# Optimization experiments

Hardware: AMD Instinct MI355X
Metric: run time of the kernel (lower is better)

The kernel has to match this reference:

```python
import jax, jax.numpy as jnp
import numpy as np

# Deterministic, fully-vectorized JAX version of the augmentation pipeline
# (labels=None branch). Randomness comes from a fixed PRNG key so the
# reference is reproducible. All per-sample PIL/CPU loops in the original
# are replaced by batched on-device ops: affine warp + hflip (geometric),
# brightness/contrast/saturation jitter (color), 3x3 gaussian blur,
# random erasing, GridMask, final clamp to [0,1].


def _affine_warp(x, key):
    """Batched inverse-mapped bilinear affine warp. x: [B,C,H,W]."""
    B, C, H, W = x.shape
    k1, k2, k3, k4 = jax.random.split(key, 4)
    deg = jnp.pi / 180.0
    ang = jax.random.uniform(k1, (B,), minval=-25.0, maxval=25.0) * deg
    shr = jax.random.uniform(k2, (B,), minval=-15.0, maxval=15.0) * deg
    scl = jax.random.uniform(k3, (B,), minval=0.85, maxval=1.15)
    trn = jax.random.uniform(k4, (B, 2), minval=-0.15, maxval=0.15)
    tx = trn[:, 0] * W
    ty = trn[:, 1] * H
    c, s = jnp.cos(ang), jnp.sin(ang)
    t = jnp.tan(shr)
    # inverse map (output pixel -> input pixel): shear^-1 @ rot^-1 / scale
    m00 = (c - t * (-s)) / scl
    m01 = (s - t * c) / scl
    m10 = (-s) / scl
    m11 = c / scl
    M = jnp.stack([jnp.stack([m00, m01], -1), jnp.stack([m10, m11], -1)], -2)  # [B,2,2]
    # centered pixel coordinate grid [2,H,W] (x, y)
    ys = jnp.arange(H, dtype=x.dtype) - (H - 1) / 2.0
    xs = jnp.arange(W, dtype=x.dtype) - (W - 1) / 2.0
    gy, gx = jnp.meshgrid(ys, xs, indexing='ij')
    grid = jnp.stack([gx, gy], 0)  # [2,H,W]
    src = jnp.einsum('bij,jhw->bihw', M, grid)  # [B,2,H,W]
    sx = src[:, 0] - tx[:, None, None] + (W - 1) / 2.0
    sy = src[:, 1] - ty[:, None, None] + (H - 1) / 2.0

    def sample_one(img, sx1, sy1):  # img [C,H,W]; sx1,sy1 [H,W]
        x0 = jnp.floor(sx1)
        y0 = jnp.floor(sy1)
        wx = sx1 - x0
        wy = sy1 - y0
        x0i = x0.astype(jnp.int32)
        y0i = y0.astype(jnp.int32)

        def g(yi, xi):
            valid = ((xi >= 0) & (xi < W) & (yi >= 0) & (yi < H)).astype(img.dtype)
            return img[:, jnp.clip(yi, 0, H - 1), jnp.clip(xi, 0, W - 1)] * valid

        return (g(y0i, x0i) * (1 - wx) * (1 - wy)
                + g(y0i, x0i + 1) * wx * (1 - wy)
                + g(y0i + 1, x0i) * (1 - wx) * wy
                + g(y0i + 1, x0i + 1) * wx * wy)

    return jax.vmap(sample_one)(x, sx, sy)


def _color_jitter(x, key):
    B = x.shape[0]
    kb, kc, ks = jax.random.split(key, 3)
    b = jax.random.uniform(kb, (B, 1, 1, 1), minval=0.7, maxval=1.3)
    c = jax.random.uniform(kc, (B, 1, 1, 1), minval=0.7, maxval=1.3)
    s = jax.random.uniform(ks, (B, 1, 1, 1), minval=0.8, maxval=1.2)
    x = x * b  # brightness
    mean = jnp.mean(x, axis=(1, 2, 3), keepdims=True)
    x = (x - mean) * c + mean  # contrast
    luma = jnp.array([0.299, 0.587, 0.114], x.dtype)
    gray = jnp.einsum('bchw,c->bhw', x, luma)[:, None]  # [B,1,H,W]
    x = gray + (x - gray) * s  # saturation
    return x


def _gaussian_blur3(x):
    C = x.shape[1]
    k1 = jnp.array([0.25, 0.5, 0.25], x.dtype)
    kern = jnp.outer(k1, k1)  # 3x3
    kern = jnp.tile(kern[None, None], (C, 1, 1, 1))  # [C,1,3,3] depthwise
    return jax.lax.conv_general_dilated(x, kern, (1, 1), 'SAME',
                                        feature_group_count=C,
                                        dimension_numbers=('NCHW', 'OIHW', 'NCHW'))


def _random_erasing(x, key):
    B, C, H, W = x.shape
    ka, kr, kt, kl, kv, kp = jax.random.split(key, 6)
    area = jax.random.uniform(ka, (B,), minval=0.02, maxval=0.1) * H * W
    ratio = jax.random.uniform(kr, (B,), minval=0.3, maxval=3.0)
    eh = jnp.clip(jnp.sqrt(area * ratio), 1, H)
    ew = jnp.clip(jnp.sqrt(area / ratio), 1, W)
    top = jax.random.uniform(kt, (B,)) * (H - eh)
    left = jax.random.uniform(kl, (B,)) * (W - ew)
    rows = jnp.arange(H, dtype=x.dtype)[None, :]
    cols = jnp.arange(W, dtype=x.dtype)[None, :]
    rmask = (rows >= top[:, None]) & (rows < (top + eh)[:, None])  # [B,H]
    cmask = (cols >= left[:, None]) & (cols < (left + ew)[:, None])  # [B,W]
    box = (rmask[:, None, :, None] & cmask[:, None, None, :])  # [B,1,H,W]
    fill = jax.random.uniform(kv, x.shape, dtype=x.dtype)  # value='random'
    apply = jax.random.bernoulli(kp, 0.3, (B, 1, 1, 1))
    return jnp.where(box & apply, fill, x)


def _grid_mask(x, key):
    B, C, H, W = x.shape
    kd, kp = jax.random.split(key)
    d = jnp.floor(jax.random.uniform(kd, (B,), minval=8.0, maxval=32.0))
    l = jnp.floor(d * 0.6)
    rows = jnp.arange(H, dtype=x.dtype)[None, :]
    cols = jnp.arange(W, dtype=x.dtype)[None, :]
    rh = jnp.mod(rows, d[:, None]) < l[:, None]  # [B,H]
    rw = jnp.mod(cols, d[:, None]) < l[:, None]  # [B,W]
    hole = rh[:, None, :, None] & rw[:, None, None, :]  # [B,1,H,W]
    apply = jax.random.bernoulli(kp, 0.3, (B, 1, 1, 1))
    return jnp.where(hole & apply, jnp.zeros_like(x), x)


def setup_inputs() -> dict:
    key = jax.random.key(0)
    x = jax.random.uniform(key, (2048, 3, 64, 64), dtype=jnp.float32)
    return {"x": x}


def reference(x) -> jnp.ndarray:
    B = x.shape[0]
    key = jax.random.key(42)
    kg, kf, kc, kb, ke, km = jax.random.split(key, 6)
    # geometric: affine warp + random horizontal flip (p=0.6)
    x = _affine_warp(x, kg)
    flip = jax.random.bernoulli(kf, 0.6, (B, 1, 1, 1))
    x = jnp.where(flip, x[..., ::-1], x)
    # color jitter
    x = _color_jitter(x, kc)
    # gaussian blur, applied per-sample with p=0.3
    blur = jax.random.bernoulli(kb, 0.3, (B, 1, 1, 1))
    x = jnp.where(blur, _gaussian_blur3(x), x)
    # random erasing
    x = _random_erasing(x, ke)
    # grid mask
    x = _grid_mask(x, km)
    return jnp.clip(x, 0.0, 1.0)
```

## Files before the change

### kernel.cpp

```cpp
#include <hip/hip_runtime.h>
#include <stdint.h>
#include <math.h>

#pragma clang fp contract(off)

struct KeyPair { uint32_t hi, lo; };
struct KTab { KeyPair k[17]; };

__host__ __device__ __forceinline__ uint32_t rotl32(uint32_t x, int r) {
  return (x << r) | (x >> (32 - r));
}

__host__ __device__ __forceinline__ void threefry2x32(uint32_t k0, uint32_t k1,
                                                      uint32_t x0, uint32_t x1,
                                                      uint32_t& o0, uint32_t& o1) {
  const uint32_t ks0 = k0, ks1 = k1, ks2 = k0 ^ k1 ^ 0x1BD11BDAu;
  x0 += ks0; x1 += ks1;
#define TF_R(r) { x0 += x1; x1 = rotl32(x1, (r)); x1 ^= x0; }
  TF_R(13) TF_R(15) TF_R(26) TF_R(6)
  x0 += ks1; x1 += ks2 + 1u;
  TF_R(17) TF_R(29) TF_R(16) TF_R(24)
  x0 += ks2; x1 += ks0 + 2u;
  TF_R(13) TF_R(15) TF_R(26) TF_R(6)
  x0 += ks0; x1 += ks1 + 3u;
  TF_R(17) TF_R(29) TF_R(16) TF_R(24)
  x0 += ks1; x1 += ks2 + 4u;
  TF_R(13) TF_R(15) TF_R(26) TF_R(6)
  x0 += ks2; x1 += ks0 + 5u;
#undef TF_R
  o0 = x0; o1 = x1;
}

__host__ __device__ __forceinline__ uint32_t jax_rbits32(KeyPair k, uint32_t i) {
  uint32_t a, b; threefry2x32(k.hi, k.lo, 0u, i, a, b);
  return a ^ b;
}

__host__ __device__ __forceinline__ KeyPair jax_split_child(KeyPair k, uint32_t j) {
  uint32_t a, b; threefry2x32(k.hi, k.lo, 0u, j, a, b);
  KeyPair r; r.hi = a; r.lo = b; return r;
}

__host__ __device__ __forceinline__ float bits_to_unit(uint32_t bits) {
  uint32_t fb = (bits >> 9) | 0x3F800000u;
  return __builtin_bit_cast(float, fb) - 1.0f;
}

__device__ __forceinline__ float map_u(float u, float mn, float mx) {
  return fmaxf(mn, u * (mx - mn) + mn);
}

__device__ __forceinline__ void gload_lds16(const float* gsrc, float* ldst) {
  __builtin_amdgcn_global_load_lds(
      (const __attribute__((address_space(1))) unsigned int*)gsrc,
      (__attribute__((address_space(3))) unsigned int*)ldst,
      16, 0, 0);
}

struct SP {
  float m00, m01, m10, m11, txp, typ;
  float bb, cc, ssat;
  float topv, t2, leftv, l2;
  float dG, lG;
  int flip, doblur, apply_e, apply_g;
};

__global__ __launch_bounds__(512, 4) void aug_kernel(const float* __restrict__ in,
                                                     float* __restrict__ out,
                                                     KTab KT, KeyPair kv, int B) {
  const int b = blockIdx.x;
  const int tid = threadIdx.x;
  __shared__ float simg[3 * 64 * 64];
  __shared__ float uarr[17];
  __shared__ SP sp;
  __shared__ unsigned long long mgrid, merow, mecol;
  __shared__ float red[8];

  const float* __restrict__ inb = in + (size_t)b * 12288;

  {
    const int wv = tid >> 6;
    const int lane = tid & 63;
#pragma unroll
    for (int it = 0; it < 6; ++it) {
      const int base = it * 2048 + wv * 256;
      gload_lds16(inb + base + 4 * lane, &simg[base]);
    }
  }

  if (tid < 17) {
    KeyPair k = KT.k[tid];
    uint32_t i = (tid == 3) ? 2u * (uint32_t)b
               : (tid == 4) ? 2u * (uint32_t)b + 1u
               : (uint32_t)b;
    uarr[tid] = bits_to_unit(jax_rbits32(k, i));
  }
  __syncthreads();

  if (tid == 0) {
    const float DEG = 0.017453292519943295f;
    float ang = map_u(uarr[0], -25.f, 25.f) * DEG;
    float shr = map_u(uarr[1], -15.f, 15.f) * DEG;
    float scl = map_u(uarr[2], 0.85f, 1.15f);
    sp.txp = map_u(uarr[3], -0.15f, 0.15f) * 64.f;
    sp.typ = map_u(uarr[4], -0.15f, 0.15f) * 64.f;
    float cA = cosf(ang), sA = sinf(ang), tS = tanf(shr);
    sp.m00 = (cA - tS * (-sA)) / scl;
    sp.m01 = (sA - tS * cA) / scl;
    sp.m10 = (-sA) / scl;
    sp.m11 = cA / scl;
    sp.flip = uarr[5] < 0.6f;
    sp.bb = map_u(uarr[6], 0.7f, 1.3f);
    sp.cc = map_u(uarr[7], 0.7f, 1.3f);
    sp.ssat = map_u(uarr[8], 0.8f, 1.2f);
    sp.doblur = uarr[9] < 0.3f;
    float area = map_u(uarr[10], 0.02f, 0.1f);
    area = area * 64.f;
    area = area * 64.f;
    float ratio = map_u(uarr[11], 0.3f, 3.0f);
    float eh = fminf(fmaxf(sqrtf(area * ratio), 1.f), 64.f);
    float ew = fminf(fmaxf(sqrtf(area / ratio), 1.f), 64.f);
    float topv = uarr[12] * (64.f - eh);
    float leftv = uarr[13] * (64.f - ew);
    sp.topv = topv; sp.t2 = topv + eh;
    sp.leftv = leftv; sp.l2 = leftv + ew;
    sp.apply_e = uarr[14] < 0.3f;
    float dG = floorf(map_u(uarr[15], 8.f, 32.f));
    sp.dG = dG;
    sp.lG = floorf(dG * 0.6f);
    sp.apply_g = uarr[16] < 0.3f;
  }
  __syncthreads();

  if (tid < 64) {
    float rf = (float)tid;
    unsigned long long g = __ballot(fmodf(rf, sp.dG) < sp.lG);
    unsigned long long er = __ballot((rf >= sp.topv) & (rf < sp.t2));
    unsigned long long ec = __ballot((rf >= sp.leftv) & (rf < sp.l2));
    if (tid == 0) { mgrid = g; merow = er; mecol = ec; }
  }
  __syncthreads();

  const float m00 = sp.m00, m01 = sp.m01, m10 = sp.m10, m11 = sp.m11;
  const float txp = sp.txp, typ = sp.typ;
  const float bb = sp.bb, cc = sp.cc, ssat = sp.ssat;
  const int flip = sp.flip, doblur = sp.doblur;
  const int apply_e = sp.apply_e, apply_g = sp.apply_g;
  const unsigned long long mg = mgrid, mer = merow, mec = mecol;

  float lsum = 0.f;
  for (int c = 0; c < 3; ++c) {
    float* plane = &simg[c * 4096];
    float vv[8];
#pragma unroll
    for (int it = 0; it < 8; ++it) {
      const int p = tid + it * 512;
      const int h = p >> 6;
      const int w = p & 63;
      const int wsrc = flip ? (63 - w) : w;
      const float gx = (float)wsrc - 31.5f;
      const float gy = (float)h - 31.5f;
      const float sx = (m00 * gx + m01 * gy) - txp + 31.5f;
      const float sy = (m10 * gx + m11 * gy) - typ + 31.5f;
      const float fx0 = floorf(sx), fy0 = floorf(sy);
      const float wx = sx - fx0, wy = sy - fy0;
      const int x0 = (int)fx0, y0 = (int)fy0;
      auto tap = [&](int yy, int xx) -> float {
        const bool v = (xx >= 0) & (xx < 64) & (yy >= 0) & (yy < 64);
        const int yc = yy < 0 ? 0 : (yy > 63 ? 63 : yy);
        const int xc = xx < 0 ? 0 : (xx > 63 ? 63 : xx);
        return v ? plane[yc * 64 + xc] : 0.f;
      };
      float v = tap(y0, x0)         * (1.f - wx) * (1.f - wy)
              + tap(y0, x0 + 1)     * wx         * (1.f - wy)
              + tap(y0 + 1, x0)     * (1.f - wx) * wy
              + tap(y0 + 1, x0 + 1) * wx         * wy;
      vv[it] = v;
      lsum += v;
    }
    if (c == 2) {
      float wsum = lsum;
      for (int off = 32; off > 0; off >>= 1) wsum += __shfl_down(wsum, off);
      if ((tid & 63) == 0) red[tid >> 6] = wsum;
    }
    __syncthreads();
#pragma unroll
    for (int it = 0; it < 8; ++it) plane[tid + it * 512] = vv[it];
  }
  __syncthreads();

  const float mean = (bb * (red[0] + red[1] + red[2] + red[3] +
                            red[4] + red[5] + red[6] + red[7])) / 12288.f;
  const float Ac = ssat * cc * bb;
  const float Gc = (1.f - ssat) * cc * bb;
  const float mprime = mean * (1.f - cc);

#pragma unroll 1
  for (int it = 0; it < 2; ++it) {
    const int qq = tid + it * 512;
    const int h = qq >> 4;
    const int w0 = (qq & 15) * 4;
    float px[3][4];
    if (doblur) {
#pragma unroll
      for (int c = 0; c < 3; ++c) {
        float win[3][6];
#pragma unroll
        for (int r = 0; r < 3; ++r) {
          const int hh = h - 1 + r;
          if (hh >= 0 && hh <= 63) {
            const float* row = &simg[c * 4096 + hh * 64];
            const float4 c4 = *(const float4*)&row[w0];
            win[r][1] = c4.x; win[r][2] = c4.y; win[r][3] = c4.z; win[r][4] = c4.w;
            win[r][0] = (w0 > 0)  ? row[w0 - 1] : 0.f;
            win[r][5] = (w0 < 60) ? row[w0 + 4] : 0.f;
          } else {
            win[r][0] = win[r][1] = win[r][2] = win[r][3] = win[r][4] = win[r][5] = 0.f;
          }
        }
#pragma unroll
        for (int j = 0; j < 4; ++j) {
          const float h0 = 0.25f * win[0][j] + 0.5f * win[0][j + 1] + 0.25f * win[0][j + 2];
          const float h1 = 0.25f * win[1][j] + 0.5f * win[1][j + 1] + 0.25f * win[1][j + 2];
          const float h2 = 0.25f * win[2][j] + 0.5f * win[2][j + 1] + 0.25f * win[2][j + 2];
          px[c][j] = 0.25f * h0 + 0.5f * h1 + 0.25f * h2;
        }
      }
    } else {
#pragma unroll
      for (int c = 0; c < 3; ++c) {
        const float4 c4 = *(const float4*)&simg[c * 4096 + h * 64 + w0];
        px[c][0] = c4.x; px[c][1] = c4.y; px[c][2] = c4.z; px[c][3] = c4.w;
      }
    }
    const float rowe = (h == 0 || h == 63) ? 0.75f : 1.f;
    const bool erow_b = apply_e && ((mer >> h) & 1ull);
    const bool grow_b = apply_g && ((mg >> h) & 1ull);
    float o[3][4];
#pragma unroll
    for (int j = 0; j < 4; ++j) {
      const int w = w0 + j;
      const float gray = 0.299f * px[0][j] + 0.587f * px[1][j] + 0.114f * px[2][j];
      float moff = mprime;
      if (doblur) {
        const float cole = (w == 0 || w == 63) ? 0.75f : 1.f;
        moff = mprime * (rowe * cole);
      }
      const bool do_er = erow_b && ((mec >> w) & 1ull);
      const bool do_gr = grow_b && ((mg >> w) & 1ull);
#pragma unroll
      for (int c = 0; c < 3; ++c) {
        float v = Ac * px[c][j] + Gc * gray + moff;
        if (do_er) {
          const uint32_t idx = ((uint32_t)(b * 3 + c) << 12) | (uint32_t)(h << 6) | (uint32_t)w;
          v = bits_to_unit(jax_rbits32(kv, idx));
        }
        if (do_gr) v = 0.f;
        o[c][j] = fminf(fmaxf(v, 0.f), 1.f);
      }
    }
#pragma unroll
    for (int c = 0; c < 3; ++c) {
      float4 st; st.x = o[c][0]; st.y = o[c][1]; st.z = o[c][2]; st.w = o[c][3];
      *(float4*)&out[(size_t)b * 12288 + c * 4096 + h * 64 + w0] = st;
    }
  }
}

extern "C" void kernel_launch(void* const* d_in, const int* in_sizes, int n_in,
                              void* d_out, int out_size, void* d_ws, size_t ws_size,
                              hipStream_t stream) {
  (void)n_in; (void)out_size; (void)d_ws; (void)ws_size;
  const float* x = (const float*)d_in[0];
  float* out = (float*)d_out;
  const int B = in_sizes[0] / (3 * 64 * 64);
  if (B <= 0) return;

  KeyPair root; root.hi = 0u; root.lo = 42u;
  KeyPair kg = jax_split_child(root, 0);
  KeyPair kf = jax_split_child(root, 1);
  KeyPair kc = jax_split_child(root, 2);
  KeyPair kb = jax_split_child(root, 3);
  KeyPair ke = jax_split_child(root, 4);
  KeyPair km = jax_split_child(root, 5);

  KTab KT;
  KT.k[0]  = jax_split_child(kg, 0);
  KT.k[1]  = jax_split_child(kg, 1);
  KT.k[2]  = jax_split_child(kg, 2);
  KT.k[3]  = jax_split_child(kg, 3);
  KT.k[4]  = KT.k[3];
  KT.k[5]  = kf;
  KT.k[6]  = jax_split_child(kc, 0);
  KT.k[7]  = jax_split_child(kc, 1);
  KT.k[8]  = jax_split_child(kc, 2);
  KT.k[9]  = kb;
  KT.k[10] = jax_split_child(ke, 0);
  KT.k[11] = jax_split_child(ke, 1);
  KT.k[12] = jax_split_child(ke, 2);
  KT.k[13] = jax_split_child(ke, 3);
  KT.k[14] = jax_split_child(ke, 5);
  KT.k[15] = jax_split_child(km, 0);
  KT.k[16] = jax_split_child(km, 1);
  KeyPair kv = jax_split_child(ke, 4);

  aug_kernel<<<dim3(B), dim3(512), 0, stream>>>(x, out, KT, kv, B);
}
```

Measured before the change: 185.3 us.

## Use zero-padded LDS image layout and fuse per-channel warp into single pass

Stores each channel in LDS with a one-pixel zero border and an odd row stride, so bilinear taps and blur windows need no bounds checks and see fewer bank conflicts. The warp now computes the coordinates once and samples all three channels, keeping results in registers and dropping the per-channel barriers. When no blur is applied, output is written straight from registers without going back through LDS. Random-parameter setup moves to one wavefront using shuffles, and global loads go through registers instead of the direct global-to-LDS path. The cost is higher register pressure (24 live warp values per thread) despite the raised occupancy hint, plus padding-based clamp logic that must exactly match the original out-of-range behaviour.

New measurement: 258.0 us. 39.2% more time.

```diff
diff --git a/kernel.cpp b/kernel.cpp
--- a/kernel.cpp
+++ b/kernel.cpp
@@ -50,94 +50,99 @@
   return fmaxf(mn, u * (mx - mn) + mn);
 }
 
-__device__ __forceinline__ void gload_lds16(const float* gsrc, float* ldst) {
-  __builtin_amdgcn_global_load_lds(
-      (const __attribute__((address_space(1))) unsigned int*)gsrc,
-      (__attribute__((address_space(3))) unsigned int*)ldst,
-      16, 0, 0);
-}
-
 struct SP {
   float m00, m01, m10, m11, txp, typ;
   float bb, cc, ssat;
-  float topv, t2, leftv, l2;
-  float dG, lG;
   int flip, doblur, apply_e, apply_g;
 };
 
-__global__ __launch_bounds__(512, 4) void aug_kernel(const float* __restrict__ in,
+#define RS  65
+#define PLS 4360
+
+__global__ __launch_bounds__(512, 6) void aug_kernel(const float* __restrict__ in,
                                                      float* __restrict__ out,
                                                      KTab KT, KeyPair kv, int B) {
   const int b = blockIdx.x;
   const int tid = threadIdx.x;
-  __shared__ float simg[3 * 64 * 64];
-  __shared__ float uarr[17];
+  __shared__ float simg[3 * PLS];
   __shared__ SP sp;
   __shared__ unsigned long long mgrid, merow, mecol;
   __shared__ float red[8];
 
   const float* __restrict__ inb = in + (size_t)b * 12288;
 
-  {
-    const int wv = tid >> 6;
-    const int lane = tid & 63;
-#pragma unroll
-    for (int it = 0; it < 6; ++it) {
-      const int base = it * 2048 + wv * 256;
-      gload_lds16(inb + base + 4 * lane, &simg[base]);
-    }
-  }
-
-  if (tid < 17) {
-    KeyPair k = KT.k[tid];
-    uint32_t i = (tid == 3) ? 2u * (uint32_t)b
-               : (tid == 4) ? 2u * (uint32_t)b + 1u
-               : (uint32_t)b;
-    uarr[tid] = bits_to_unit(jax_rbits32(k, i));
-  }
-  __syncthreads();
-
-  if (tid == 0) {
+  float4 st[6];
+#pragma unroll
+  for (int it = 0; it < 6; ++it) st[it] = ((const float4*)inb)[tid + it * 512];
+
+  if (tid < 64) {
+    float myu = 0.f;
+    if (tid < 17) {
+      KeyPair k = KT.k[tid];
+      uint32_t i = (tid == 3) ? 2u * (uint32_t)b
+                 : (tid == 4) ? 2u * (uint32_t)b + 1u
+                 : (uint32_t)b;
+      myu = bits_to_unit(jax_rbits32(k, i));
+    }
+    float u[17];
+#pragma unroll
+    for (int j = 0; j < 17; ++j) u[j] = __shfl(myu, j);
+
     const float DEG = 0.017453292519943295f;
-    float ang = map_u(uarr[0], -25.f, 25.f) * DEG;
-    float shr = map_u(uarr[1], -15.f, 15.f) * DEG;
-    float scl = map_u(uarr[2], 0.85f, 1.15f);
-    sp.txp = map_u(uarr[3], -0.15f, 0.15f) * 64.f;
-    sp.typ = map_u(uarr[4], -0.15f, 0.15f) * 64.f;
-    float cA = cosf(ang), sA = sinf(ang), tS = tanf(shr);
-    sp.m00 = (cA - tS * (-sA)) / scl;
-    sp.m01 = (sA - tS * cA) / scl;
-    sp.m10 = (-sA) / scl;
-    sp.m11 = cA / scl;
-    sp.flip = uarr[5] < 0.6f;
-    sp.bb = map_u(uarr[6], 0.7f, 1.3f);
-    sp.cc = map_u(uarr[7], 0.7f, 1.3f);
-    sp.ssat = map_u(uarr[8], 0.8f, 1.2f);
-    sp.doblur = uarr[9] < 0.3f;
-    float area = map_u(uarr[10], 0.02f, 0.1f);
+    const float ang = map_u(u[0], -25.f, 25.f) * DEG;
+    const float shr = map_u(u[1], -15.f, 15.f) * DEG;
+    const float scl = map_u(u[2], 0.85f, 1.15f);
+    const float t_x = map_u(u[3], -0.15f, 0.15f) * 64.f;
+    const float t_y = map_u(u[4], -0.15f, 0.15f) * 64.f;
+    const float cA = cosf(ang), sA = sinf(ang), tS = tanf(shr);
+    float area = map_u(u[10], 0.02f, 0.1f);
     area = area * 64.f;
     area = area * 64.f;
-    float ratio = map_u(uarr[11], 0.3f, 3.0f);
-    float eh = fminf(fmaxf(sqrtf(area * ratio), 1.f), 64.f);
-    float ew = fminf(fmaxf(sqrtf(area / ratio), 1.f), 64.f);
-    float topv = uarr[12] * (64.f - eh);
-    float leftv = uarr[13] * (64.f - ew);
-    sp.topv = topv; sp.t2 = topv + eh;
-    sp.leftv = leftv; sp.l2 = leftv + ew;
-    sp.apply_e = uarr[14] < 0.3f;
-    float dG = floorf(map_u(uarr[15], 8.f, 32.f));
-    sp.dG = dG;
-    sp.lG = floorf(dG * 0.6f);
-    sp.apply_g = uarr[16] < 0.3f;
-  }
-  __syncthreads();
-
-  if (tid < 64) {
-    float rf = (float)tid;
-    unsigned long long g = __ballot(fmodf(rf, sp.dG) < sp.lG);
-    unsigned long long er = __ballot((rf >= sp.topv) & (rf < sp.t2));
-    unsigned long long ec = __ballot((rf >= sp.leftv) & (rf < sp.l2));
-    if (tid == 0) { mgrid = g; merow = er; mecol = ec; }
+    const float ratio = map_u(u[11], 0.3f, 3.0f);
+    const float eh = fminf(fmaxf(sqrtf(area * ratio), 1.f), 64.f);
+    const float ew = fminf(fmaxf(sqrtf(area / ratio), 1.f), 64.f);
+    const float topv = u[12] * (64.f - eh);
+    const float leftv = u[13] * (64.f - ew);
+    const float dG = floorf(map_u(u[15], 8.f, 32.f));
+    const float lG = floorf(dG * 0.6f);
+
+    const float rf = (float)tid;
+    const unsigned long long g  = __ballot(fmodf(rf, dG) < lG);
+    const unsigned long long er = __ballot((rf >= topv) & (rf < (topv + eh)));
+    const unsigned long long ec = __ballot((rf >= leftv) & (rf < (leftv + ew)));
+    if (tid == 0) {
+      sp.m00 = (cA - tS * (-sA)) / scl;
+      sp.m01 = (sA - tS * cA) / scl;
+      sp.m10 = (-sA) / scl;
+      sp.m11 = cA / scl;
+      sp.txp = t_x; sp.typ = t_y;
+      sp.flip = u[5] < 0.6f;
+      sp.bb = map_u(u[6], 0.7f, 1.3f);
+      sp.cc = map_u(u[7], 0.7f, 1.3f);
+      sp.ssat = map_u(u[8], 0.8f, 1.2f);
+      sp.doblur = u[9] < 0.3f;
+      sp.apply_e = u[14] < 0.3f;
+      sp.apply_g = u[16] < 0.3f;
+      mgrid = g; merow = er; mecol = ec;
+    }
+  } else if (tid < 328) {
+    const int z = tid - 64;
+    int a;
+    if (z < 65)       a = z;
+    else if (z < 200) a = 4160 + z;
+    else              a = (z - 199) * RS;
+#pragma unroll
+    for (int c = 0; c < 3; ++c) simg[c * PLS + a] = 0.f;
+  }
+
+#pragma unroll
+  for (int it = 0; it < 6; ++it) {
+    const int f = it * 2048 + tid * 4;
+    const int c = f >> 12;
+    const int r = (f >> 6) & 63;
+    const int cc = f & 63;
+    float* d = &simg[c * PLS + (r + 1) * RS + cc + 1];
+    d[0] = st[it].x; d[1] = st[it].y; d[2] = st[it].z; d[3] = st[it].w;
   }
   __syncthreads();
 
@@ -148,44 +153,37 @@
   const int apply_e = sp.apply_e, apply_g = sp.apply_g;
   const unsigned long long mg = mgrid, mer = merow, mec = mecol;
 
+  float vv[3][8];
   float lsum = 0.f;
-  for (int c = 0; c < 3; ++c) {
-    float* plane = &simg[c * 4096];
-    float vv[8];
-#pragma unroll
-    for (int it = 0; it < 8; ++it) {
-      const int p = tid + it * 512;
-      const int h = p >> 6;
-      const int w = p & 63;
-      const int wsrc = flip ? (63 - w) : w;
-      const float gx = (float)wsrc - 31.5f;
-      const float gy = (float)h - 31.5f;
-      const float sx = (m00 * gx + m01 * gy) - txp + 31.5f;
-      const float sy = (m10 * gx + m11 * gy) - typ + 31.5f;
-      const float fx0 = floorf(sx), fy0 = floorf(sy);
-      const float wx = sx - fx0, wy = sy - fy0;
-      const int x0 = (int)fx0, y0 = (int)fy0;
-      auto tap = [&](int yy, int xx) -> float {
-        const bool v = (xx >= 0) & (xx < 64) & (yy >= 0) & (yy < 64);
-        const int yc = yy < 0 ? 0 : (yy > 63 ? 63 : yy);
-        const int xc = xx < 0 ? 0 : (xx > 63 ? 63 : xx);
-        return v ? plane[yc * 64 + xc] : 0.f;
-      };
-      float v = tap(y0, x0)         * (1.f - wx) * (1.f - wy)
-              + tap(y0, x0 + 1)     * wx         * (1.f - wy)
-              + tap(y0 + 1, x0)     * (1.f - wx) * wy
-              + tap(y0 + 1, x0 + 1) * wx         * wy;
-      vv[it] = v;
+#pragma unroll
+  for (int it = 0; it < 8; ++it) {
+    const int p = tid + it * 512;
+    const int h = p >> 6;
+    const int w = p & 63;
+    const int wsrc = flip ? (63 - w) : w;
+    const float gx = (float)wsrc - 31.5f;
+    const float gy = (float)h - 31.5f;
+    float sx = (m00 * gx + m01 * gy) - txp + 31.5f;
+    float sy = (m10 * gx + m11 * gy) - typ + 31.5f;
+    sx = fminf(fmaxf(sx, -1.f), 64.f);
+    sy = fminf(fmaxf(sy, -1.f), 64.f);
+    const float fx0 = floorf(sx), fy0 = floorf(sy);
+    const float wx = sx - fx0, wy = sy - fy0;
+    const float omx = 1.f - wx, omy = 1.f - wy;
+    const float w00 = omx * omy, w01 = wx * omy, w10 = omx * wy, w11 = wx * wy;
+    const int a = ((int)fy0 + 1) * RS + (int)fx0 + 1;
+#pragma unroll
+    for (int c = 0; c < 3; ++c) {
+      const float* t = &simg[c * PLS + a];
+      const float v = t[0] * w00 + t[1] * w01 + t[RS] * w10 + t[RS + 1] * w11;
+      vv[c][it] = v;
       lsum += v;
     }
-    if (c == 2) {
-      float wsum = lsum;
-      for (int off = 32; off > 0; off >>= 1) wsum += __shfl_down(wsum, off);
-      if ((tid & 63) == 0) red[tid >> 6] = wsum;
-    }
-    __syncthreads();
-#pragma unroll
-    for (int it = 0; it < 8; ++it) plane[tid + it * 512] = vv[it];
+  }
+  {
+    float wsum = lsum;
+    for (int off = 32; off > 0; off >>= 1) wsum += __shfl_down(wsum, off);
+    if ((tid & 63) == 0) red[tid >> 6] = wsum;
   }
   __syncthreads();
 
@@ -194,29 +192,50 @@
   const float Ac = ssat * cc * bb;
   const float Gc = (1.f - ssat) * cc * bb;
   const float mprime = mean * (1.f - cc);
-
+  float* __restrict__ ob = out + (size_t)b * 12288;
+
+  if (!doblur) {
+#pragma unroll
+    for (int it = 0; it < 8; ++it) {
+      const int p = tid + it * 512;
+      const int h = p >> 6, w = p & 63;
+      const bool do_er = apply_e && ((mer >> h) & 1ull) && ((mec >> w) & 1ull);
+      const bool do_gr = apply_g && ((mg >> h) & 1ull) && ((mg >> w) & 1ull);
+      const float gray = 0.299f * vv[0][it] + 0.587f * vv[1][it] + 0.114f * vv[2][it];
+#pragma unroll
+      for (int c = 0; c < 3; ++c) {
+        float v = Ac * vv[c][it] + Gc * gray + mprime;
+        if (do_er) {
+          const uint32_t idx = ((uint32_t)(b * 3 + c) << 12) | (uint32_t)p;
+          v = bits_to_unit(jax_rbits32(kv, idx));
+        }
+        if (do_gr) v = 0.f;
+        ob[c * 4096 + p] = fminf(fmaxf(v, 0.f), 1.f);
+      }
+    }
+  } else {
+#pragma unroll
+    for (int it = 0; it < 8; ++it) {
+      const int p = tid + it * 512;
+      const int a = ((p >> 6) + 1) * RS + (p & 63) + 1;
+#pragma unroll
+      for (int c = 0; c < 3; ++c) simg[c * PLS + a] = vv[c][it];
+    }
+    __syncthreads();
 #pragma unroll 1
-  for (int it = 0; it < 2; ++it) {
-    const int qq = tid + it * 512;
-    const int h = qq >> 4;
-    const int w0 = (qq & 15) * 4;
-    float px[3][4];
-    if (doblur) {
+    for (int it = 0; it < 2; ++it) {
+      const int qq = tid + it * 512;
+      const int h = qq >> 4;
+      const int w0 = (qq & 15) * 4;
+      float px[3][4];
 #pragma unroll
       for (int c = 0; c < 3; ++c) {
         float win[3][6];
 #pragma unroll
         for (int r = 0; r < 3; ++r) {
-          const int hh = h - 1 + r;
-          if (hh >= 0 && hh <= 63) {
-            const float* row = &simg[c * 4096 + hh * 64];
-            const float4 c4 = *(const float4*)&row[w0];
-            win[r][1] = c4.x; win[r][2] = c4.y; win[r][3] = c4.z; win[r][4] = c4.w;
-            win[r][0] = (w0 > 0)  ? row[w0 - 1] : 0.f;
-            win[r][5] = (w0 < 60) ? row[w0 + 4] : 0.f;
-          } else {
-            win[r][0] = win[r][1] = win[r][2] = win[r][3] = win[r][4] = win[r][5] = 0.f;
-          }
+          const float* row = &simg[c * PLS + (h + r) * RS + w0];
+#pragma unroll
+          for (int k = 0; k < 6; ++k) win[r][k] = row[k];
         }
 #pragma unroll
         for (int j = 0; j < 4; ++j) {
@@ -226,43 +245,34 @@
           px[c][j] = 0.25f * h0 + 0.5f * h1 + 0.25f * h2;
         }
       }
-    } else {
+      const float rowe = (h == 0 || h == 63) ? 0.75f : 1.f;
+      const bool erow_b = apply_e && ((mer >> h) & 1ull);
+      const bool grow_b = apply_g && ((mg >> h) & 1ull);
+      float o[3][4];
+#pragma unroll
+      for (int j = 0; j < 4; ++j) {
+        const int w = w0 + j;
+        const float gray = 0.299f * px[0][j] + 0.587f * px[1][j] + 0.114f * px[2][j];
+        const float cole = (w == 0 || w == 63) ? 0.75f : 1.f;
+        const float moff = mprime * (rowe * cole);
+        const bool do_er = erow_b && ((mec >> w) & 1ull);
+        const bool do_gr = grow_b && ((mg >> w) & 1ull);
+#pragma unroll
+        for (int c = 0; c < 3; ++c) {
+          float v = Ac * px[c][j] + Gc * gray + moff;
+          if (do_er) {
+            const uint32_t idx = ((uint32_t)(b * 3 + c) << 12) | (uint32_t)(h << 6) | (uint32_t)w;
+            v = bits_to_unit(jax_rbits32(kv, idx));
+          }
+          if (do_gr) v = 0.f;
+          o[c][j] = fminf(fmaxf(v, 0.f), 1.f);
+        }
+      }
 #pragma unroll
       for (int c = 0; c < 3; ++c) {
-        const float4 c4 = *(const float4*)&simg[c * 4096 + h * 64 + w0];
-        px[c][0] = c4.x; px[c][1] = c4.y; px[c][2] = c4.z; px[c][3] = c4.w;
+        float4 stv; stv.x = o[c][0]; stv.y = o[c][1]; stv.z = o[c][2]; stv.w = o[c][3];
+        *(float4*)&ob[c * 4096 + h * 64 + w0] = stv;
       }
-    }
-    const float rowe = (h == 0 || h == 63) ? 0.75f : 1.f;
-    const bool erow_b = apply_e && ((mer >> h) & 1ull);
-    const bool grow_b = apply_g && ((mg >> h) & 1ull);
-    float o[3][4];
-#pragma unroll
-    for (int j = 0; j < 4; ++j) {
-      const int w = w0 + j;
-      const float gray = 0.299f * px[0][j] + 0.587f * px[1][j] + 0.114f * px[2][j];
-      float moff = mprime;
-      if (doblur) {
-        const float cole = (w == 0 || w == 63) ? 0.75f : 1.f;
-        moff = mprime * (rowe * cole);
-      }
-      const bool do_er = erow_b && ((mec >> w) & 1ull);
-      const bool do_gr = grow_b && ((mg >> w) & 1ull);
-#pragma unroll
-      for (int c = 0; c < 3; ++c) {
-        float v = Ac * px[c][j] + Gc * gray + moff;
-        if (do_er) {
-          const uint32_t idx = ((uint32_t)(b * 3 + c) << 12) | (uint32_t)(h << 6) | (uint32_t)w;
-          v = bits_to_unit(jax_rbits32(kv, idx));
-        }
-        if (do_gr) v = 0.f;
-        o[c][j] = fminf(fmaxf(v, 0.f), 1.f);
-      }
-    }
-#pragma unroll
-    for (int c = 0; c < 3; ++c) {
-      float4 st; st.x = o[c][0]; st.y = o[c][1]; st.z = o[c][2]; st.w = o[c][3];
-      *(float4*)&out[(size_t)b * 12288 + c * 4096 + h * 64 + w0] = st;
     }
   }
 }
```
